# Kernel optimization log

Measured on AMD Instinct MI355X. Metric: run time of the kernel, lower is better.

## Reference

```python
import jax, jax.numpy as jnp
import numpy as np
import math

D_MODEL = 1024
NHEAD = 16
D_K = D_MODEL // NHEAD
LAMDA_ATT = 1.0
B, L = 2, 2048


def setup_inputs() -> dict:
    key = jax.random.key(0)
    ks = jax.random.split(key, 10)
    s = 1.0 / math.sqrt(D_MODEL)
    x = jax.random.normal(ks[0], (B, L, D_MODEL), dtype=jnp.float32)
    delta_r = jax.random.uniform(ks[1], (B, L), dtype=jnp.float32)  # positive, fed to log
    Wq = jax.random.normal(ks[2], (D_MODEL, D_MODEL), dtype=jnp.float32) * s
    Wk = jax.random.normal(ks[3], (D_MODEL, D_MODEL), dtype=jnp.float32) * s
    Wv = jax.random.normal(ks[4], (D_MODEL, D_MODEL), dtype=jnp.float32) * s
    Wo = jax.random.normal(ks[5], (D_MODEL, D_MODEL), dtype=jnp.float32) * s
    bq = jnp.zeros((D_MODEL,), jnp.float32)
    bk = jnp.zeros((D_MODEL,), jnp.float32)
    bv = jnp.zeros((D_MODEL,), jnp.float32)
    bo = jnp.zeros((D_MODEL,), jnp.float32)
    return {"x": x, "delta_r": delta_r, "Wq": Wq, "bq": bq, "Wk": Wk, "bk": bk,
            "Wv": Wv, "bv": bv, "Wo": Wo, "bo": bo}


def reference(x, delta_r, Wq, bq, Wk, bk, Wv, bv, Wo, bo):
    b, l, d = x.shape
    h, dk = NHEAD, D_K

    def proj(y, W, bias):
        # [B,L,D] -> [B,H,L,dk]
        return (y @ W + bias).reshape(b, l, h, dk).transpose(0, 2, 1, 3)

    v_scaled = x * delta_r[..., None]
    q = proj(x, Wq, bq)
    k = proj(x, Wk, bk)
    v = proj(v_scaled, Wv, bv)

    scores = jnp.einsum('bhqd,bhkd->bhqk', q, k) / math.sqrt(dk)
    pos = jnp.arange(l)
    dist = jnp.abs(pos[None, :] - pos[:, None]).astype(scores.dtype)  # [L,L]
    rel_bias = LAMDA_ATT * jnp.log(delta_r + 1e-6)  # [B,L]
    scores = scores - dist[None, None] * 0.1 + rel_bias[:, None, None, :]

    attn = jax.nn.softmax(scores, axis=-1)  # dropout is identity in eval mode
    context = jnp.einsum('bhqk,bhkd->bqhd', attn, v).reshape(b, l, d)
    out = context @ Wo + bo
    return out, attn.mean(axis=1)
```

## Files before the change

kernel.cpp:

```cpp
#include <hip/hip_runtime.h>
#include <math.h>

#define DMODEL 1024
#define NHEAD  16
#define DK     64
#define BB     2
#define LL     2048
#define MTOT   (BB*LL)

#define LOG2E      1.4426950408889634f
#define SCQ        (0.125f * LOG2E)
#define C2LOG      (0.1f * LOG2E)
#define SKIP_BOUND (-24.0f)

typedef __bf16 bf16_t;
typedef __bf16 bf16x8 __attribute__((ext_vector_type(8)));
typedef __bf16 bf16x4 __attribute__((ext_vector_type(4)));
typedef float  f32x4  __attribute__((ext_vector_type(4)));

static __device__ __forceinline__ f32x4 mfma16(bf16x8 a, bf16x8 b, f32x4 c) {
    return __builtin_amdgcn_mfma_f32_16x16x32_bf16(a, b, c, 0, 0, 0);
}
static __device__ __forceinline__ float exp2f_fast(float x) {
    return __builtin_amdgcn_exp2f(x);
}
static __device__ __forceinline__ float log2f_fast(float x) {
    return __builtin_amdgcn_logf(x);
}
static __device__ __forceinline__ void gl_lds16(const bf16_t* g, bf16_t* l) {
    __builtin_amdgcn_global_load_lds(
        (const __attribute__((address_space(1))) unsigned int*)g,
        (__attribute__((address_space(3))) unsigned int*)l, 16, 0, 0);
}

__global__ __launch_bounds__(256) void prep_fused_k(
    const float* __restrict__ x, const float* __restrict__ dr,
    bf16_t* __restrict__ xb, float* __restrict__ logd2,
    const float* __restrict__ Wq, const float* __restrict__ Wk,
    const float* __restrict__ Wv, const float* __restrict__ Wo,
    bf16_t* __restrict__ Wcat, bf16_t* __restrict__ Wot)
{
    __shared__ __align__(16) float Ts[64][68];
    const int bid = blockIdx.x;
    const int tid = threadIdx.x;
    if (bid < 2048) {
        size_t gid = (size_t)bid * 256 + tid;
        size_t off = gid * 8;
        float4 a = *(const float4*)(x + off);
        float4 c = *(const float4*)(x + off + 4);
        float va[8] = {a.x, a.y, a.z, a.w, c.x, c.y, c.z, c.w};
        bf16x8 o1;
#pragma unroll
        for (int j = 0; j < 8; ++j) o1[j] = (bf16_t)va[j];
        *(bf16x8*)(xb + off) = o1;
        if (gid < MTOT) logd2[gid] = log2f_fast(dr[gid] + 1e-6f);
    } else {
        const int t = bid - 2048;
        const int z = t >> 8;
        const float* W = (z == 0) ? Wq : (z == 1) ? Wk : (z == 2) ? Wv : Wo;
        bf16_t* dst = (z < 3) ? (Wcat + (size_t)z * DMODEL * DMODEL) : Wot;
        const int k0 = (t & 15) * 64, n0 = ((t >> 4) & 15) * 64;
#pragma unroll
        for (int i = 0; i < 4; ++i) {
            int u = tid + 256 * i, r = u >> 4, c4 = (u & 15) * 4;
            *(float4*)&Ts[r][c4] = *(const float4*)(W + (size_t)(k0 + r) * DMODEL + n0 + c4);
        }
        __syncthreads();
#pragma unroll
        for (int i = 0; i < 2; ++i) {
            int u = tid + 256 * i, n = u >> 3, k8 = (u & 7) * 8;
            bf16x8 v;
#pragma unroll
            for (int j = 0; j < 8; ++j) v[j] = (bf16_t)Ts[k8 + j][n];
            *(bf16x8*)(dst + (size_t)(n0 + n) * DMODEL + k0 + k8) = v;
        }
    }
}

__global__ __launch_bounds__(256, 3) void gemm128_k(
    const bf16_t* __restrict__ A, const bf16_t* __restrict__ Bt,
    const float* __restrict__ b0, const float* __restrict__ b1,
    const float* __restrict__ b2, const float* __restrict__ delta,
    float* __restrict__ outf, bf16_t* __restrict__ outQ,
    bf16_t* __restrict__ outK, bf16_t* __restrict__ outVt, int mode)
{
    __shared__ __align__(16) bf16_t Asw[128 * 64];
    __shared__ __align__(16) bf16_t Bsw[128 * 64];
    const int tid = threadIdx.x, lane = tid & 63, w = tid >> 6;
    const int quad = lane >> 4, n16 = lane & 15;
    const int wm = (w & 1) * 64, wn = (w >> 1) * 64;
    const int m0 = blockIdx.y * 128, n0 = blockIdx.x * 128;
    const int srow = lane >> 3;
    const int scb  = (lane & 7) ^ srow;

    f32x4 acc[4][4] = {};

    for (int K0 = 0; K0 < DMODEL; K0 += 64) {
        __syncthreads();
#pragma unroll
        for (int i = 0; i < 4; ++i) {
            int rb = w * 32 + i * 8;
            gl_lds16(A  + (size_t)(m0 + rb + srow) * DMODEL + K0 + scb * 8,
                     &Asw[rb * 64]);
            gl_lds16(Bt + (size_t)(n0 + rb + srow) * DMODEL + K0 + scb * 8,
                     &Bsw[rb * 64]);
        }
        __syncthreads();
#pragma unroll
        for (int kc = 0; kc < 2; ++kc) {
            const int pcb = ((kc * 4 + quad) ^ (n16 & 7)) * 8;
            bf16x8 af[4], bfv[4];
#pragma unroll
            for (int mi = 0; mi < 4; ++mi)
                af[mi] = *(const bf16x8*)&Asw[(wm + mi * 16 + n16) * 64 + pcb];
#pragma unroll
            for (int ni = 0; ni < 4; ++ni)
                bfv[ni] = *(const bf16x8*)&Bsw[(wn + ni * 16 + n16) * 64 + pcb];
#pragma unroll
            for (int mi = 0; mi < 4; ++mi)
#pragma unroll
                for (int ni = 0; ni < 4; ++ni)
                    acc[mi][ni] = mfma16(af[mi], bfv[ni], acc[mi][ni]);
        }
    }

    if (mode == 0) {
        const int region = n0 >> 10;
        if (region == 2) {
#pragma unroll
            for (int mi = 0; mi < 4; ++mi) {
                const int mbase = m0 + wm + mi * 16 + quad * 4;
                const int bidx = mbase >> 11, l = mbase & (LL - 1);
                const f32x4 dm4 = *(const f32x4*)(delta + mbase);
#pragma unroll
                for (int ni = 0; ni < 4; ++ni) {
                    const int nl = (n0 & 1023) + wn + ni * 16 + n16;
                    const int h = nl >> 6, dd = nl & 63;
                    const float bv = b2[nl];
                    bf16x4 pk;
#pragma unroll
                    for (int r = 0; r < 4; ++r)
                        pk[r] = (bf16_t)(acc[mi][ni][r] * dm4[r] + bv);
                    *(bf16x4*)(outVt + ((size_t)(bidx * NHEAD + h) * DK + dd) * LL + l) = pk;
                }
            }
        } else {
            const float* bias = (region == 0) ? b0 : b1;
            bf16_t* dst = (region == 0) ? outQ : outK;
            const float qs = (region == 0) ? SCQ : 1.0f;
#pragma unroll
            for (int mi = 0; mi < 4; ++mi) {
#pragma unroll
                for (int r = 0; r < 4; ++r) {
                    const int m = m0 + wm + mi * 16 + quad * 4 + r;
                    const int bidx = m >> 11, l = m & (LL - 1);
#pragma unroll
                    for (int ni = 0; ni < 4; ++ni) {
                        const int nl = (n0 & 1023) + wn + ni * 16 + n16;
                        const int h = nl >> 6, dd = nl & 63;
                        float v = (acc[mi][ni][r] + bias[nl]) * qs;
                        dst[(((size_t)(bidx * NHEAD + h) * LL) + l) * DK + dd] = (bf16_t)v;
                    }
                }
            }
        }
    } else {
#pragma unroll
        for (int mi = 0; mi < 4; ++mi) {
#pragma unroll
            for (int r = 0; r < 4; ++r) {
                const int m = m0 + wm + mi * 16 + quad * 4 + r;
#pragma unroll
                for (int ni = 0; ni < 4; ++ni) {
                    const int n = n0 + wn + ni * 16 + n16;
                    outf[(size_t)m * DMODEL + n] = acc[mi][ni][r] + b0[n];
                }
            }
        }
    }
}

__global__ __launch_bounds__(256) void stats_k(
    const bf16_t* __restrict__ Q, const bf16_t* __restrict__ K,
    const float* __restrict__ logd2, float* __restrict__ Qn,
    float* __restrict__ Kn, float* __restrict__ dlb, float* __restrict__ ldx)
{
    __shared__ float qn_s[256], kn_s[256], dg_s[256];
    const int blk = blockIdx.x;
    const int bh = blk >> 3, seg = blk & 7, b = bh >> 4;
    const int tid = threadIdx.x;
    const int row = seg * 256 + tid;
    const size_t base = (size_t)bh * LL * DK;

    float qn2 = 0.f, kn2 = 0.f, dg = 0.f;
#pragma unroll
    for (int j = 0; j < 8; ++j) {
        bf16x8 qv = *(const bf16x8*)(Q + base + (size_t)row * DK + j * 8);
        bf16x8 kv = *(const bf16x8*)(K + base + (size_t)row * DK + j * 8);
#pragma unroll
        for (int e = 0; e < 8; ++e) {
            float fq = (float)qv[e], fk = (float)kv[e];
            qn2 += fq * fq; kn2 += fk * fk; dg += fq * fk;
        }
    }
    qn_s[tid] = qn2;
    kn_s[tid] = kn2;
    dg_s[tid] = dg + logd2[b * LL + row];
    __syncthreads();

    if (tid < 2) {
        float mq = 0.f, md = 1e30f;
        for (int r = 0; r < 128; ++r) {
            mq = fmaxf(mq, qn_s[tid * 128 + r]);
            md = fminf(md, dg_s[tid * 128 + r]);
        }
        Qn[bh * 16 + seg * 2 + tid] = sqrtf(mq);
        dlb[bh * 16 + seg * 2 + tid] = md;
    } else if (tid >= 64 && tid < 68) {
        const int t = tid - 64;
        float mk = 0.f;
        for (int r = 0; r < 64; ++r) mk = fmaxf(mk, kn_s[t * 64 + r]);
        Kn[bh * 32 + seg * 4 + t] = sqrtf(mk);
    } else if (tid >= 128 && tid < 132 && (bh & 15) == 0) {
        const int t = tid - 128;
        float ml = -1e30f;
        for (int r = 0; r < 64; ++r)
            ml = fmaxf(ml, logd2[b * LL + seg * 256 + t * 64 + r]);
        ldx[b * 32 + seg * 4 + t] = ml;
    }
}

__global__ __launch_bounds__(256) void mlstat_k(
    const float* __restrict__ mlws, float* __restrict__ mlmin)
{
    __shared__ float s[2048];
    const int tid = threadIdx.x, bh = blockIdx.x;
#pragma unroll
    for (int i = 0; i < 8; ++i)
        s[tid + 256 * i] = mlws[(size_t)bh * LL + tid + 256 * i];
    __syncthreads();
    if (tid < 16) {
        float m = 1e30f;
        for (int r = 0; r < 128; ++r) m = fminf(m, s[tid * 128 + r]);
        mlmin[bh * 16 + tid] = m;
    }
}

__global__ __launch_bounds__(256, 4) void attn_flash_mfma_k(
    const bf16_t* __restrict__ Q, const bf16_t* __restrict__ K,
    const bf16_t* __restrict__ Vt, const float* __restrict__ logd2,
    const float* __restrict__ Qn, const float* __restrict__ Kn,
    const float* __restrict__ dlb, const float* __restrict__ ldx,
    bf16_t* __restrict__ ctx, float* __restrict__ mlout)
{
    __shared__ __align__(16) bf16_t Ks[64][72];
    __shared__ __align__(16) bf16_t Vts[64][72];
    __shared__ __align__(16) bf16_t Ps[4][16][72];
    __shared__ float logds[64];

    const int tid = threadIdx.x;
    const int lane = tid & 63, w = tid >> 6;
    const int quad = lane >> 4, n16 = lane & 15;
    const int bh = blockIdx.x, b = bh >> 4, h = bh & 15;
    const int qt = blockIdx.y, q0 = qt * 64;
    const size_t base = (size_t)bh * LL * DK;
    const int q = q0 + w * 16 + n16;

    bf16x8 qa[2];
#pragma unroll
    for (int kc = 0; kc < 2; ++kc)
        qa[kc] = *(const bf16x8*)(Q + base + (size_t)q * DK + kc * 32 + quad * 8);

    unsigned mask = 0;
    {
        const float qn = Qn[bh * 16 + (qt >> 1)], dl = dlb[bh * 16 + (qt >> 1)];
        for (int t = 0; t < 32; ++t) {
            const int kc0 = t * 64;
            const int dmin = (kc0 > q0 + 63) ? (kc0 - (q0 + 63))
                           : ((q0 > kc0 + 63) ? (q0 - (kc0 + 63)) : 0);
            const float bound = qn * Kn[bh * 32 + t] + ldx[b * 32 + t]
                              - C2LOG * (float)dmin - dl;
            if (bound > SKIP_BOUND) mask |= (1u << t);
        }
    }

    const int strow = tid >> 3, stc8 = (tid & 7) * 8;
    bf16x8 kr0, kr1, vr0, vr1;
    float ldr = 0.f;
    auto prefetch = [&](int k0) {
        kr0 = *(const bf16x8*)(K + base + (size_t)(k0 + strow) * DK + stc8);
        kr1 = *(const bf16x8*)(K + base + (size_t)(k0 + 32 + strow) * DK + stc8);
        vr0 = *(const bf16x8*)(Vt + base + (size_t)strow * LL + k0 + stc8);
        vr1 = *(const bf16x8*)(Vt + base + (size_t)(32 + strow) * LL + k0 + stc8);
        if (tid < 64) ldr = logd2[b * LL + k0 + tid];
    };

    float m_c = -1e30f, l_c = 0.f;
    f32x4 o[4] = {};
    const float dfq = (float)(q - quad * 4);

    int t = (int)__builtin_ctz(mask);
    prefetch(t * 64);
    for (;;) {
        const unsigned rem = (t < 31) ? (mask >> (t + 1)) : 0u;
        const int tn = rem ? (t + 1 + (int)__builtin_ctz(rem)) : -1;
        __syncthreads();
        *(bf16x8*)&Ks[strow][stc8]       = kr0;
        *(bf16x8*)&Ks[32 + strow][stc8]  = kr1;
        *(bf16x8*)&Vts[strow][stc8]      = vr0;
        *(bf16x8*)&Vts[32 + strow][stc8] = vr1;
        if (tid < 64) logds[tid] = ldr;
        __syncthreads();
        if (tn >= 0) prefetch(tn * 64);
        const int k0 = t * 64;

        f32x4 s[4] = {};
#pragma unroll
        for (int kc = 0; kc < 2; ++kc) {
#pragma unroll
            for (int kt = 0; kt < 4; ++kt) {
                bf16x8 kb = *(const bf16x8*)&Ks[kt * 16 + n16][kc * 32 + quad * 8];
                s[kt] = mfma16(kb, qa[kc], s[kt]);
            }
        }
        const float df = dfq - (float)k0;
#pragma unroll
        for (int kt = 0; kt < 4; ++kt) {
            f32x4 ldv = *(const f32x4*)&logds[kt * 16 + quad * 4];
#pragma unroll
            for (int r = 0; r < 4; ++r)
                s[kt][r] += ldv[r] - C2LOG * fabsf(df - (float)(kt * 16 + r));
        }
        f32x4 mx;
#pragma unroll
        for (int r = 0; r < 4; ++r)
            mx[r] = fmaxf(fmaxf(s[0][r], s[1][r]), fmaxf(s[2][r], s[3][r]));
        float rm = fmaxf(fmaxf(mx[0], mx[1]), fmaxf(mx[2], mx[3]));
        rm = fmaxf(rm, __shfl_xor(rm, 16));
        rm = fmaxf(rm, __shfl_xor(rm, 32));
        const float mn = fmaxf(m_c, rm);
        const float alpha = exp2f_fast(m_c - mn);
        if (__any(mn > m_c)) {
#pragma unroll
            for (int dt = 0; dt < 4; ++dt)
#pragma unroll
                for (int r = 0; r < 4; ++r) o[dt][r] *= alpha;
        }
        f32x4 ps = {0.f, 0.f, 0.f, 0.f};
#pragma unroll
        for (int kt = 0; kt < 4; ++kt)
#pragma unroll
            for (int r = 0; r < 4; ++r) {
                float p = exp2f_fast(s[kt][r] - mn);
                s[kt][r] = p;
                ps[r] += p;
            }
        float psum = (ps[0] + ps[1]) + (ps[2] + ps[3]);
        psum += __shfl_xor(psum, 16);
        psum += __shfl_xor(psum, 32);
        l_c = l_c * alpha + psum;
        m_c = mn;
#pragma unroll
        for (int kt = 0; kt < 4; ++kt) {
            bf16x4 pk;
#pragma unroll
            for (int r = 0; r < 4; ++r) pk[r] = (bf16_t)s[kt][r];
            *(bf16x4*)&Ps[w][n16][kt * 16 + quad * 4] = pk;
        }
        __threadfence_block();
#pragma unroll
        for (int kc = 0; kc < 2; ++kc) {
            bf16x8 pa = *(const bf16x8*)&Ps[w][n16][kc * 32 + quad * 8];
#pragma unroll
            for (int dt = 0; dt < 4; ++dt) {
                bf16x8 vb = *(const bf16x8*)&Vts[dt * 16 + n16][kc * 32 + quad * 8];
                o[dt] = mfma16(vb, pa, o[dt]);
            }
        }
        if (tn < 0) break;
        t = tn;
    }
    const float inv = 1.f / l_c;
#pragma unroll
    for (int dt = 0; dt < 4; ++dt) {
        bf16x4 ov;
#pragma unroll
        for (int r = 0; r < 4; ++r) ov[r] = (bf16_t)(o[dt][r] * inv);
        *(bf16x4*)(ctx + ((size_t)b * LL + q) * DMODEL + h * DK +
                   dt * 16 + quad * 4) = ov;
    }
    if (quad == 0)
        mlout[(size_t)bh * LL + q] = m_c + log2f_fast(l_c);
}

__global__ __launch_bounds__(256, 3) void tail_fused_k(
    const bf16_t* __restrict__ A, const bf16_t* __restrict__ Bt,
    const float* __restrict__ b0, float* __restrict__ outf,
    const bf16_t* __restrict__ Q, const bf16_t* __restrict__ K,
    const float* __restrict__ logd2, const float* __restrict__ mlws,
    const float* __restrict__ Qn, const float* __restrict__ Kn,
    const float* __restrict__ mlmin, const float* __restrict__ ldx,
    float* __restrict__ outmean)
{
    __shared__ __align__(16) char smem[24576];

    const int bid = blockIdx.x;
    const int tid = threadIdx.x;
    const int lane = tid & 63, w = tid >> 6;
    const int quad = lane >> 4, n16 = lane & 15;

    if (bid < 512) {
        bf16_t* Asw = (bf16_t*)smem;
        bf16_t* Bsw = (bf16_t*)(smem + 8192);
        const int wm = (w & 1) * 32, wn = (w >> 1) * 64;
        const int m0 = (bid >> 3) * 64, n0 = (bid & 7) * 128;
        const int srow = lane >> 3;
        const int scb  = (lane & 7) ^ srow;

        f32x4 acc[2][4] = {};

        for (int K0 = 0; K0 < DMODEL; K0 += 64) {
            __syncthreads();
#pragma unroll
            for (int i = 0; i < 2; ++i) {
                int rb = w * 16 + i * 8;
                gl_lds16(A + (size_t)(m0 + rb + srow) * DMODEL + K0 + scb * 8,
                         &Asw[rb * 64]);
            }
#pragma unroll
            for (int i = 0; i < 4; ++i) {
                int rb = w * 32 + i * 8;
                gl_lds16(Bt + (size_t)(n0 + rb + srow) * DMODEL + K0 + scb * 8,
                         &Bsw[rb * 64]);
            }
            __syncthreads();
#pragma unroll
            for (int kc = 0; kc < 2; ++kc) {
                const int pcb = ((kc * 4 + quad) ^ (n16 & 7)) * 8;
                bf16x8 af[2], bfv[4];
#pragma unroll
                for (int mi = 0; mi < 2; ++mi)
                    af[mi] = *(const bf16x8*)&Asw[(wm + mi * 16 + n16) * 64 + pcb];
#pragma unroll
                for (int ni = 0; ni < 4; ++ni)
                    bfv[ni] = *(const bf16x8*)&Bsw[(wn + ni * 16 + n16) * 64 + pcb];
#pragma unroll
                for (int mi = 0; mi < 2; ++mi)
#pragma unroll
                    for (int ni = 0; ni < 4; ++ni)
                        acc[mi][ni] = mfma16(af[mi], bfv[ni], acc[mi][ni]);
            }
        }
#pragma unroll
        for (int mi = 0; mi < 2; ++mi) {
#pragma unroll
            for (int r = 0; r < 4; ++r) {
                const int m = m0 + wm + mi * 16 + quad * 4 + r;
#pragma unroll
                for (int ni = 0; ni < 4; ++ni) {
                    const int n = n0 + wn + ni * 16 + n16;
                    outf[(size_t)m * DMODEL + n] = acc[mi][ni][r] + b0[n];
                }
            }
        }
        return;
    }

    typedef bf16_t KsRow[64][72];
    KsRow* Ks = (KsRow*)smem;
    float (*mls)[128] = (float(*)[128])(smem + 18432);
    float* logds = (float*)(smem + 19456);

    const int tb = bid - 512;
    const int k0 = (tb & 31) * 64, q0 = ((tb >> 5) & 15) * 128, b = tb >> 9;
    const int qq[2] = {q0 + w * 32 + n16, q0 + w * 32 + 16 + n16};

    if (tid < 64) logds[tid] = logd2[b * LL + k0 + tid];
    __syncthreads();

    float bias0[2][4][4];
#pragma unroll
    for (int qg = 0; qg < 2; ++qg) {
        const float df = (float)(qq[qg] - k0 - quad * 4);
#pragma unroll
        for (int kt = 0; kt < 4; ++kt) {
            f32x4 ldv = *(const f32x4*)&logds[kt * 16 + quad * 4];
#pragma unroll
            for (int r = 0; r < 4; ++r)
                bias0[qg][kt][r] = ldv[r] - C2LOG * fabsf(df - (float)(kt * 16 + r));
        }
    }

    const int qt = q0 >> 7, ktl = k0 >> 6;
    const int dmin = (k0 > q0 + 127) ? (k0 - (q0 + 127))
                   : ((q0 > k0 + 63) ? (q0 - (k0 + 63)) : 0);
    unsigned hmask = 0;
    {
        const float dterm = ldx[b * 32 + ktl] - C2LOG * (float)dmin;
        for (int h = 0; h < NHEAD; ++h) {
            const int bh = b * 16 + h;
            const float bound = Qn[bh * 16 + qt] * Kn[bh * 32 + ktl] + dterm
                              - mlmin[bh * 16 + qt];
            if (bound > SKIP_BOUND) hmask |= (1u << h);
        }
    }

    f32x4 acc[2][4] = {};

    if (hmask) {
        const int strow = tid >> 3, stc8 = (tid & 7) * 8;
        bf16x8 kr0, kr1, qan[2][2];
        float mlv = 0.f;
        auto load_head = [&](int h) {
            const size_t hb = (size_t)(b * NHEAD + h) * LL * DK;
            kr0 = *(const bf16x8*)(K + hb + (size_t)(k0 + strow) * DK + stc8);
            kr1 = *(const bf16x8*)(K + hb + (size_t)(k0 + 32 + strow) * DK + stc8);
#pragma unroll
            for (int qg = 0; qg < 2; ++qg)
#pragma unroll
                for (int kc = 0; kc < 2; ++kc)
                    qan[qg][kc] = *(const bf16x8*)(Q + hb + (size_t)qq[qg] * DK +
                                                   kc * 32 + quad * 8);
            if (tid < 128) mlv = mlws[(size_t)(b * NHEAD + h) * LL + q0 + tid];
        };

        int h = (int)__builtin_ctz(hmask);
        load_head(h);
        int pc = 0;
        for (;;) {
            const unsigned rem = (h < 15) ? (hmask >> (h + 1)) : 0u;
            const int hn = rem ? (h + 1 + (int)__builtin_ctz(rem)) : -1;
            const int p = pc & 1;
            *(bf16x8*)&Ks[p][strow][stc8]      = kr0;
            *(bf16x8*)&Ks[p][32 + strow][stc8] = kr1;
            if (tid < 128) mls[p][tid] = mlv;
            bf16x8 qc[2][2] = {{qan[0][0], qan[0][1]}, {qan[1][0], qan[1][1]}};
            __syncthreads();
            if (hn >= 0) load_head(hn);

            f32x4 s[2][4] = {};
#pragma unroll
            for (int kc = 0; kc < 2; ++kc) {
#pragma unroll
                for (int kt = 0; kt < 4; ++kt) {
                    bf16x8 kb = *(const bf16x8*)&Ks[p][kt * 16 + n16][kc * 32 + quad * 8];
                    s[0][kt] = mfma16(kb, qc[0][kc], s[0][kt]);
                    s[1][kt] = mfma16(kb, qc[1][kc], s[1][kt]);
                }
            }
#pragma unroll
            for (int qg = 0; qg < 2; ++qg) {
                const float ml = mls[p][w * 32 + qg * 16 + n16];
#pragma unroll
                for (int kt = 0; kt < 4; ++kt)
#pragma unroll
                    for (int r = 0; r < 4; ++r)
                        acc[qg][kt][r] += exp2f_fast(s[qg][kt][r] +
                                                     bias0[qg][kt][r] - ml);
            }
            ++pc;
            if (hn < 0) break;
            h = hn;
        }
    }

    const float invH = 1.f / (float)NHEAD;
#pragma unroll
    for (int qg = 0; qg < 2; ++qg)
#pragma unroll
        for (int kt = 0; kt < 4; ++kt) {
            f32x4 ov;
#pragma unroll
            for (int r = 0; r < 4; ++r) ov[r] = acc[qg][kt][r] * invH;
            *(f32x4*)(outmean + ((size_t)b * LL + qq[qg]) * LL + k0 +
                      kt * 16 + quad * 4) = ov;
        }
}

extern "C" void kernel_launch(void* const* d_in, const int* in_sizes, int n_in,
                              void* d_out, int out_size, void* d_ws, size_t ws_size,
                              hipStream_t stream) {
    const float* x  = (const float*)d_in[0];
    const float* dr = (const float*)d_in[1];
    const float* Wq = (const float*)d_in[2];
    const float* bq = (const float*)d_in[3];
    const float* Wk = (const float*)d_in[4];
    const float* bk = (const float*)d_in[5];
    const float* Wv = (const float*)d_in[6];
    const float* bv = (const float*)d_in[7];
    const float* Wo = (const float*)d_in[8];
    const float* bo = (const float*)d_in[9];
    float* out = (float*)d_out;
    char* ws = (char*)d_ws;
    const size_t MB = 1ull << 20;

    bf16_t* xb   = (bf16_t*)(ws);
    bf16_t* Wcat = (bf16_t*)(ws + 8 * MB);
    bf16_t* Wot  = (bf16_t*)(ws + 14 * MB);
    bf16_t* Qb   = (bf16_t*)(ws + 16 * MB);
    bf16_t* Kb   = (bf16_t*)(ws + 24 * MB);
    bf16_t* Vtb  = (bf16_t*)(ws + 32 * MB);
    float*  logd = (float*)(ws + 40 * MB);
    float*  mlws = (float*)(ws + 41 * MB);
    float*  Qns  = (float*)(ws + 42 * MB);
    float*  Kns  = (float*)(ws + 42 * MB + 4096);
    float*  dlb  = (float*)(ws + 42 * MB + 12288);
    float*  ldxp = (float*)(ws + 42 * MB + 16384);
    float*  mlmn = (float*)(ws + 42 * MB + 20480);
    bf16_t* ctx  = xb;

    prep_fused_k<<<3072, 256, 0, stream>>>(x, dr, xb, logd,
                                           Wq, Wk, Wv, Wo, Wcat, Wot);

    gemm128_k<<<dim3(24, 32), 256, 0, stream>>>(xb, Wcat, bq, bk, bv, dr,
                                                nullptr, Qb, Kb, Vtb, 0);
    stats_k<<<256, 256, 0, stream>>>(Qb, Kb, logd, Qns, Kns, dlb, ldxp);

    attn_flash_mfma_k<<<dim3(32, 32), 256, 0, stream>>>(Qb, Kb, Vtb, logd,
                                                        Qns, Kns, dlb, ldxp,
                                                        ctx, mlws);
    mlstat_k<<<32, 256, 0, stream>>>(mlws, mlmn);
    tail_fused_k<<<1536, 256, 0, stream>>>(ctx, Wot, bo, out,
                                           Qb, Kb, logd, mlws, Qns, Kns,
                                           mlmn, ldxp,
                                           out + (size_t)MTOT * DMODEL);
}
```

Measured before the change: 219.6 us.

## Reorder tail blocks by diagonal distance and load K/Q directly from global

Attention-mean blocks now come first in the grid, and the output-projection GEMM blocks move to the end. Within each query tile, key tiles are assigned in order of increasing distance from the diagonal, so the blocks that do heavy work are dispatched early. The LDS double-buffered K staging, the per-head barriers and the shared log-delta buffer are removed in favour of direct global/L1 loads into registers. This trades fewer barriers and less LDS traffic for redundant global loads across waves and less latency hiding between heads.

```diff
diff --git a/kernel.cpp b/kernel.cpp
--- a/kernel.cpp
+++ b/kernel.cpp
@@ -409,11 +409,12 @@
     const int lane = tid & 63, w = tid >> 6;
     const int quad = lane >> 4, n16 = lane & 15;
 
-    if (bid < 512) {
+    if (bid >= 1024) {
         bf16_t* Asw = (bf16_t*)smem;
         bf16_t* Bsw = (bf16_t*)(smem + 8192);
+        const int gb = bid - 1024;
         const int wm = (w & 1) * 32, wn = (w >> 1) * 64;
-        const int m0 = (bid >> 3) * 64, n0 = (bid & 7) * 128;
+        const int m0 = (gb >> 3) * 64, n0 = (gb & 7) * 128;
         const int srow = lane >> 3;
         const int scb  = (lane & 7) ^ srow;
 
@@ -466,17 +467,26 @@
         return;
     }
 
-    typedef bf16_t KsRow[64][72];
-    KsRow* Ks = (KsRow*)smem;
-    float (*mls)[128] = (float(*)[128])(smem + 18432);
-    float* logds = (float*)(smem + 19456);
-
-    const int tb = bid - 512;
-    const int k0 = (tb & 31) * 64, q0 = ((tb >> 5) & 15) * 128, b = tb >> 9;
+    const int q0 = ((bid >> 5) & 15) * 128, b = bid >> 9;
+
+    int ktile = 0;
+    {
+        const int c = q0 >> 6;
+        int want = bid & 31;
+        for (int d = 0; d < 32; ++d) {
+            int ka = c - d, kb2 = c + 1 + d;
+            if (ka >= 0 && ka < 32) {
+                if (want == 0) { ktile = ka; break; }
+                --want;
+            }
+            if (kb2 >= 0 && kb2 < 32) {
+                if (want == 0) { ktile = kb2; break; }
+                --want;
+            }
+        }
+    }
+    const int k0 = ktile * 64;
     const int qq[2] = {q0 + w * 32 + n16, q0 + w * 32 + 16 + n16};
-
-    if (tid < 64) logds[tid] = logd2[b * LL + k0 + tid];
-    __syncthreads();
 
     float bias0[2][4][4];
 #pragma unroll
@@ -484,22 +494,22 @@
         const float df = (float)(qq[qg] - k0 - quad * 4);
 #pragma unroll
         for (int kt = 0; kt < 4; ++kt) {
-            f32x4 ldv = *(const f32x4*)&logds[kt * 16 + quad * 4];
+            const f32x4 ldv = *(const f32x4*)(logd2 + b * LL + k0 + kt * 16 + quad * 4);
 #pragma unroll
             for (int r = 0; r < 4; ++r)
                 bias0[qg][kt][r] = ldv[r] - C2LOG * fabsf(df - (float)(kt * 16 + r));
         }
     }
 
-    const int qt = q0 >> 7, ktl = k0 >> 6;
+    const int qt = q0 >> 7;
     const int dmin = (k0 > q0 + 127) ? (k0 - (q0 + 127))
                    : ((q0 > k0 + 63) ? (q0 - (k0 + 63)) : 0);
     unsigned hmask = 0;
     {
-        const float dterm = ldx[b * 32 + ktl] - C2LOG * (float)dmin;
+        const float dterm = ldx[b * 32 + ktile] - C2LOG * (float)dmin;
         for (int h = 0; h < NHEAD; ++h) {
             const int bh = b * 16 + h;
-            const float bound = Qn[bh * 16 + qt] * Kn[bh * 32 + ktl] + dterm
+            const float bound = Qn[bh * 16 + qt] * Kn[bh * 32 + ktile] + dterm
                               - mlmin[bh * 16 + qt];
             if (bound > SKIP_BOUND) hmask |= (1u << h);
         }
@@ -508,57 +518,41 @@
     f32x4 acc[2][4] = {};
 
     if (hmask) {
-        const int strow = tid >> 3, stc8 = (tid & 7) * 8;
-        bf16x8 kr0, kr1, qan[2][2];
-        float mlv = 0.f;
-        auto load_head = [&](int h) {
-            const size_t hb = (size_t)(b * NHEAD + h) * LL * DK;
-            kr0 = *(const bf16x8*)(K + hb + (size_t)(k0 + strow) * DK + stc8);
-            kr1 = *(const bf16x8*)(K + hb + (size_t)(k0 + 32 + strow) * DK + stc8);
-#pragma unroll
-            for (int qg = 0; qg < 2; ++qg)
-#pragma unroll
-                for (int kc = 0; kc < 2; ++kc)
-                    qan[qg][kc] = *(const bf16x8*)(Q + hb + (size_t)qq[qg] * DK +
-                                                   kc * 32 + quad * 8);
-            if (tid < 128) mlv = mlws[(size_t)(b * NHEAD + h) * LL + q0 + tid];
-        };
-
         int h = (int)__builtin_ctz(hmask);
-        load_head(h);
-        int pc = 0;
         for (;;) {
             const unsigned rem = (h < 15) ? (hmask >> (h + 1)) : 0u;
             const int hn = rem ? (h + 1 + (int)__builtin_ctz(rem)) : -1;
-            const int p = pc & 1;
-            *(bf16x8*)&Ks[p][strow][stc8]      = kr0;
-            *(bf16x8*)&Ks[p][32 + strow][stc8] = kr1;
-            if (tid < 128) mls[p][tid] = mlv;
-            bf16x8 qc[2][2] = {{qan[0][0], qan[0][1]}, {qan[1][0], qan[1][1]}};
-            __syncthreads();
-            if (hn >= 0) load_head(hn);
+            const size_t hb = (size_t)(b * NHEAD + h) * LL * DK;
+
+            const float ml0 = mlws[(size_t)(b * NHEAD + h) * LL + qq[0]];
+            const float ml1 = mlws[(size_t)(b * NHEAD + h) * LL + qq[1]];
 
             f32x4 s[2][4] = {};
 #pragma unroll
             for (int kc = 0; kc < 2; ++kc) {
+                bf16x8 kbf[4];
+#pragma unroll
+                for (int kt = 0; kt < 4; ++kt)
+                    kbf[kt] = *(const bf16x8*)(K + hb +
+                              (size_t)(k0 + kt * 16 + n16) * DK + kc * 32 + quad * 8);
+                const bf16x8 qc0 = *(const bf16x8*)(Q + hb + (size_t)qq[0] * DK +
+                                                    kc * 32 + quad * 8);
+                const bf16x8 qc1 = *(const bf16x8*)(Q + hb + (size_t)qq[1] * DK +
+                                                    kc * 32 + quad * 8);
 #pragma unroll
                 for (int kt = 0; kt < 4; ++kt) {
-                    bf16x8 kb = *(const bf16x8*)&Ks[p][kt * 16 + n16][kc * 32 + quad * 8];
-                    s[0][kt] = mfma16(kb, qc[0][kc], s[0][kt]);
-                    s[1][kt] = mfma16(kb, qc[1][kc], s[1][kt]);
+                    s[0][kt] = mfma16(kbf[kt], qc0, s[0][kt]);
+                    s[1][kt] = mfma16(kbf[kt], qc1, s[1][kt]);
                 }
             }
 #pragma unroll
-            for (int qg = 0; qg < 2; ++qg) {
-                const float ml = mls[p][w * 32 + qg * 16 + n16];
-#pragma unroll
-                for (int kt = 0; kt < 4; ++kt)
-#pragma unroll
-                    for (int r = 0; r < 4; ++r)
-                        acc[qg][kt][r] += exp2f_fast(s[qg][kt][r] +
-                                                     bias0[qg][kt][r] - ml);
-            }
-            ++pc;
+            for (int kt = 0; kt < 4; ++kt) {
+#pragma unroll
+                for (int r = 0; r < 4; ++r) {
+                    acc[0][kt][r] += exp2f_fast(s[0][kt][r] + bias0[0][kt][r] - ml0);
+                    acc[1][kt][r] += exp2f_fast(s[1][kt][r] + bias0[1][kt][r] - ml1);
+                }
+            }
             if (hn < 0) break;
             h = hn;
         }
```

Measured after the change: 297.5 us. 1.35x slower.
